# Kernel tuning notes

Measured on AMD Instinct MI355X. Metric: run time of the kernel, lower is better.

## Reference

```python
import jax, jax.numpy as jnp
import numpy as np

TOP_K = 2
NEG_INF = -1e30


def setup_inputs() -> dict:
    key = jax.random.key(0)
    ks = jax.random.split(key, 9)
    S, B, D, H, E, O = 2, 2048, 1024, 2048, 8, 1024
    return {
        "xs": jax.random.normal(ks[0], (S, B, D), jnp.float32),
        "Wg": jax.random.normal(ks[1], (D, E), jnp.float32),
        "b": jax.random.normal(ks[2], (E,), jnp.float32),
        "fc1_w": jax.random.normal(ks[3], (E, H, D), jnp.float32) * 0.02,
        "fc1_b": jax.random.normal(ks[4], (E, H), jnp.float32) * 0.02,
        "fc2_w": jax.random.normal(ks[5], (E, H, H), jnp.float32) * 0.02,
        "fc2_b": jax.random.normal(ks[6], (E, H), jnp.float32) * 0.02,
        "final_w": jax.random.normal(ks[7], (O, H), jnp.float32) * 0.02,
        "final_b": jax.random.normal(ks[8], (O,), jnp.float32) * 0.02,
    }


def reference(xs, Wg, b, fc1_w, fc1_b, fc2_w, fc2_b, final_w, final_b):
    # xs: [S, B, D] stacked x_list
    S = xs.shape[0]
    # gate logits H: [S, B, E]
    Hg = jnp.einsum('sbd,de->sbe', xs, Wg) + b
    expert_probs = jax.nn.softmax(Hg, axis=-1)  # per-view full softmax
    # top-k threshold mask (H >= kth largest value)
    topk_vals = jax.lax.top_k(Hg, TOP_K)[0]          # [S, B, K]
    thr = topk_vals[..., -1:]                         # [S, B, 1]
    H_masked = jnp.where(Hg >= thr, Hg, NEG_INF)
    G = jax.nn.softmax(H_masked, axis=-1)             # [S, B, E]
    # dense all-expert FFN: [S, B, E, H]
    h = jnp.einsum('sbd,ehd->sbeh', xs, fc1_w) + fc1_b
    h = jax.nn.relu(h)
    eo = jnp.einsum('sbeh,egh->sbeg', h, fc2_w) + fc2_b
    # gated sum over experts, averaged over views: [B, H]
    combined = jnp.einsum('sbe,sbeh->bh', G, eo) / S
    out = combined @ final_w.T + final_b               # [B, O]
    return out, expert_probs
```

## Files before the change

kernel.cpp:

```cpp
#include <hip/hip_runtime.h>
#include <stdint.h>

#define S_DIM 2
#define B_DIM 2048
#define D_DIM 1024
#define H_DIM 2048
#define E_DIM 8
#define O_DIM 1024
#define NTOK 4096
#define CAP 12288

typedef __attribute__((ext_vector_type(8))) short bf16x8;
typedef __attribute__((ext_vector_type(4))) float f32x4;

__device__ __forceinline__ unsigned short f2bf(float f) {
    union { float f; uint32_t i; } c; c.f = f;
    uint32_t r = c.i + 0x7FFFu + ((c.i >> 16) & 1u);
    return (unsigned short)(r >> 16);
}
__device__ __forceinline__ float bf2f(unsigned short u) {
    union { uint32_t i; float f; } c; c.i = (uint32_t)u << 16;
    return c.f;
}
__device__ __forceinline__ uint32_t pack2(float a, float b) {
    return (uint32_t)f2bf(a) | ((uint32_t)f2bf(b) << 16);
}
__device__ __forceinline__ void stage8(const float* __restrict__ src,
                                       unsigned short* __restrict__ dst) {
    float4 f0 = *(const float4*)src;
    float4 f1 = *(const float4*)(src + 4);
    int4 v;
    v.x = (int)pack2(f0.x, f0.y);
    v.y = (int)pack2(f0.z, f0.w);
    v.z = (int)pack2(f1.x, f1.y);
    v.w = (int)pack2(f1.z, f1.w);
    *(int4*)dst = v;
}

__device__ __forceinline__ void glds16(const unsigned short* g, unsigned short* l) {
    __builtin_amdgcn_global_load_lds(
        (__attribute__((address_space(1))) void*)g,
        (__attribute__((address_space(3))) void*)l,
        16, 0, 0);
}

__global__ __launch_bounds__(256) void convert_kernel(
    const float* __restrict__ src, unsigned short* __restrict__ dst, int n8)
{
    int i = blockIdx.x * blockDim.x + threadIdx.x;
    if (i < n8) stage8(src + (size_t)i * 8, dst + (size_t)i * 8);
}

__global__ __launch_bounds__(256) void gating_kernel(
    const float* __restrict__ xs,
    const float* __restrict__ Wg,
    const float* __restrict__ bvec,
    float* __restrict__ probs_out,
    int* __restrict__ counts,
    int* __restrict__ sel_cnt,
    int* __restrict__ sel_e,
    float* __restrict__ sel_g,
    unsigned short* __restrict__ xs_bf)
{
    const int wave = threadIdx.x >> 6;
    const int lane = threadIdx.x & 63;
    const int t = blockIdx.x * 4 + wave;
    const float* x = xs + (size_t)t * D_DIM;

    float acc[8];
#pragma unroll
    for (int e = 0; e < 8; ++e) acc[e] = 0.f;

#pragma unroll
    for (int i = 0; i < D_DIM / 64; ++i) {
        int d = i * 64 + lane;
        float xv = x[d];
        xs_bf[(size_t)t * D_DIM + d] = f2bf(xv);
        float4 w0 = *(const float4*)(Wg + (size_t)d * 8);
        float4 w1 = *(const float4*)(Wg + (size_t)d * 8 + 4);
        acc[0] += xv * w0.x; acc[1] += xv * w0.y;
        acc[2] += xv * w0.z; acc[3] += xv * w0.w;
        acc[4] += xv * w1.x; acc[5] += xv * w1.y;
        acc[6] += xv * w1.z; acc[7] += xv * w1.w;
    }
#pragma unroll
    for (int off = 32; off > 0; off >>= 1) {
#pragma unroll
        for (int e = 0; e < 8; ++e)
            acc[e] += __shfl_down(acc[e], off);
    }

    if (lane == 0) {
        float Hg[8];
#pragma unroll
        for (int e = 0; e < 8; ++e) Hg[e] = acc[e] + bvec[e];

        int a1 = 0;
#pragma unroll
        for (int e = 1; e < 8; ++e) if (Hg[e] > Hg[a1]) a1 = e;
        float m1 = Hg[a1];
        float m2 = -1e30f;
#pragma unroll
        for (int e = 0; e < 8; ++e) if (e != a1 && Hg[e] > m2) m2 = Hg[e];

        float ex[8]; float sum = 0.f;
#pragma unroll
        for (int e = 0; e < 8; ++e) { ex[e] = expf(Hg[e] - m1); sum += ex[e]; }
        float inv = 1.f / sum;
#pragma unroll
        for (int e = 0; e < 8; ++e)
            probs_out[(size_t)t * 8 + e] = ex[e] * inv;

        float den = 0.f;
#pragma unroll
        for (int e = 0; e < 8; ++e) if (Hg[e] >= m2) den += ex[e];
        float invd = 1.f / den;
        int n = 0;
#pragma unroll
        for (int e = 0; e < 8; ++e) {
            if (Hg[e] >= m2) {
                sel_e[t * 8 + n] = e;
                sel_g[t * 8 + n] = ex[e] * invd;
                ++n;
                atomicAdd(&counts[e], 1);
            }
        }
        sel_cnt[t] = n;
    }
}

__global__ void scan_kernel(const int* __restrict__ counts, int* __restrict__ offsets)
{
    if (threadIdx.x == 0) {
        int tot = 0;
#pragma unroll
        for (int e = 0; e < 8; ++e) { offsets[e] = tot; tot += counts[e]; }
    }
}

__global__ __launch_bounds__(256) void scatter_kernel(
    const int* __restrict__ sel_cnt,
    const int* __restrict__ sel_e,
    const float* __restrict__ sel_g,
    const int* __restrict__ offsets,
    int* __restrict__ cursors,
    int* __restrict__ pair_token,
    float* __restrict__ pair_gate,
    int* __restrict__ tok_slot)
{
    int t = blockIdx.x * blockDim.x + threadIdx.x;
    if (t >= NTOK) return;
    int n = sel_cnt[t];
    for (int i = 0; i < n && i < 8; ++i) {
        int e = sel_e[t * 8 + i];
        int r = atomicAdd(&cursors[e], 1);
        int slot = offsets[e] + r;
        if (slot < CAP) {
            pair_token[slot] = t;
            pair_gate[slot]  = sel_g[t * 8 + i];
            tok_slot[t * 8 + i] = slot;
        } else {
            tok_slot[t * 8 + i] = -1;
        }
    }
}


__global__ __launch_bounds__(256, 2) void fc1_kernel(
    const unsigned short* __restrict__ xs_bf,
    const unsigned short* __restrict__ fc1_wb,
    const float* __restrict__ fc1_b,
    const int* __restrict__ counts,
    const int* __restrict__ offsets,
    const int* __restrict__ pair_token,
    unsigned short* __restrict__ h)
{
    const int wg = blockIdx.x;
    const int e = wg & 7;
    const int idx = wg >> 3;
    const int mtile = idx >> 3;
    const int ntile = idx & 7;
    const int cnt = counts[e];
    if (mtile * 128 >= cnt) return;
    const int offs = offsets[e];

    __shared__ __align__(16) unsigned short As[128 * 64];
    __shared__ __align__(16) unsigned short Bs[256 * 64];

    const int tid  = threadIdx.x;
    const int lane = tid & 63;
    const int wid  = tid >> 6;
    const int lrow = lane & 15;
    const int kq   = lane >> 4;
    const int swz  = lrow & 7;

    const unsigned short* aSrc[4];
    int aDst[4];
#pragma unroll
    for (int i = 0; i < 4; ++i) {
        int c = i * 256 + tid;
        int row = c >> 3;
        int gran = (c & 7) ^ (row & 7);
        int m = mtile * 128 + row;
        int mc = m < cnt ? m : cnt - 1;
        int tok = pair_token[offs + mc];
        aSrc[i] = xs_bf + (size_t)tok * D_DIM + gran * 8;
        aDst[i] = (i * 256 + wid * 64) * 8;
    }
    const unsigned short* bSrc[8];
    int bDst[8];
#pragma unroll
    for (int i = 0; i < 8; ++i) {
        int c = i * 256 + tid;
        int row = c >> 3;
        int gran = (c & 7) ^ (row & 7);
        int n = ntile * 256 + row;
        bSrc[i] = fc1_wb + ((size_t)e * H_DIM + n) * D_DIM + gran * 8;
        bDst[i] = (i * 256 + wid * 64) * 8;
    }

    f32x4 acc[8][4];
#pragma unroll
    for (int i = 0; i < 8; ++i)
#pragma unroll
        for (int j = 0; j < 4; ++j)
            acc[i][j] = (f32x4){0.f, 0.f, 0.f, 0.f};

    for (int k0 = 0; k0 < D_DIM; k0 += 64) {
        __syncthreads();
#pragma unroll
        for (int i = 0; i < 4; ++i) glds16(aSrc[i] + k0, &As[aDst[i]]);
#pragma unroll
        for (int i = 0; i < 8; ++i) glds16(bSrc[i] + k0, &Bs[bDst[i]]);
        __syncthreads();
#pragma unroll
        for (int ks = 0; ks < 2; ++ks) {
            const int sg = ((ks * 4 + kq) ^ swz) * 8;
            bf16x8 af[8], bfr[4];
#pragma unroll
            for (int i = 0; i < 8; ++i)
                af[i] = *(const bf16x8*)&As[(i * 16 + lrow) * 64 + sg];
#pragma unroll
            for (int j = 0; j < 4; ++j)
                bfr[j] = *(const bf16x8*)&Bs[(wid * 64 + j * 16 + lrow) * 64 + sg];
#pragma unroll
            for (int i = 0; i < 8; ++i)
#pragma unroll
                for (int j = 0; j < 4; ++j)
                    acc[i][j] = __builtin_amdgcn_mfma_f32_16x16x32_bf16(
                        af[i], bfr[j], acc[i][j], 0, 0, 0);
        }
    }

    int ncol[4]; float bias[4];
#pragma unroll
    for (int j = 0; j < 4; ++j) {
        ncol[j] = ntile * 256 + wid * 64 + j * 16 + lrow;
        bias[j] = fc1_b[e * H_DIM + ncol[j]];
    }
#pragma unroll
    for (int i = 0; i < 8; ++i) {
#pragma unroll
        for (int r = 0; r < 4; ++r) {
            int m = mtile * 128 + i * 16 + kq * 4 + r;
            if (m < cnt) {
                size_t base = (size_t)(offs + m) * H_DIM;
#pragma unroll
                for (int j = 0; j < 4; ++j) {
                    float v = acc[i][j][r] + bias[j];
                    h[base + ncol[j]] = f2bf(v > 0.f ? v : 0.f);
                }
            }
        }
    }
}

__global__ __launch_bounds__(256, 2) void fc2_kernel(
    const unsigned short* __restrict__ h,
    const unsigned short* __restrict__ fc2_wb,
    const float* __restrict__ fc2_b,
    const int* __restrict__ counts,
    const int* __restrict__ offsets,
    const float* __restrict__ pair_gate,
    unsigned short* __restrict__ eo_bf)
{
    const int wg = blockIdx.x;
    const int e = wg & 7;
    const int idx = wg >> 3;
    const int mtile = idx >> 3;
    const int ntile = idx & 7;
    const int cnt = counts[e];
    if (mtile * 128 >= cnt) return;
    const int offs = offsets[e];

    __shared__ __align__(16) unsigned short As[128 * 64];
    __shared__ __align__(16) unsigned short Bs[256 * 64];

    const int tid  = threadIdx.x;
    const int lane = tid & 63;
    const int wid  = tid >> 6;
    const int lrow = lane & 15;
    const int kq   = lane >> 4;
    const int swz  = lrow & 7;

    const unsigned short* aSrc[4];
    int aDst[4];
#pragma unroll
    for (int i = 0; i < 4; ++i) {
        int c = i * 256 + tid;
        int row = c >> 3;
        int gran = (c & 7) ^ (row & 7);
        int m = mtile * 128 + row;
        int mc = m < cnt ? m : cnt - 1;
        aSrc[i] = h + (size_t)(offs + mc) * H_DIM + gran * 8;
        aDst[i] = (i * 256 + wid * 64) * 8;
    }
    const unsigned short* bSrc[8];
    int bDst[8];
#pragma unroll
    for (int i = 0; i < 8; ++i) {
        int c = i * 256 + tid;
        int row = c >> 3;
        int gran = (c & 7) ^ (row & 7);
        int n = ntile * 256 + row;
        bSrc[i] = fc2_wb + ((size_t)e * H_DIM + n) * H_DIM + gran * 8;
        bDst[i] = (i * 256 + wid * 64) * 8;
    }

    f32x4 acc[8][4];
#pragma unroll
    for (int i = 0; i < 8; ++i)
#pragma unroll
        for (int j = 0; j < 4; ++j)
            acc[i][j] = (f32x4){0.f, 0.f, 0.f, 0.f};

    for (int k0 = 0; k0 < H_DIM; k0 += 64) {
        __syncthreads();
#pragma unroll
        for (int i = 0; i < 4; ++i) glds16(aSrc[i] + k0, &As[aDst[i]]);
#pragma unroll
        for (int i = 0; i < 8; ++i) glds16(bSrc[i] + k0, &Bs[bDst[i]]);
        __syncthreads();
#pragma unroll
        for (int ks = 0; ks < 2; ++ks) {
            const int sg = ((ks * 4 + kq) ^ swz) * 8;
            bf16x8 af[8], bfr[4];
#pragma unroll
            for (int i = 0; i < 8; ++i)
                af[i] = *(const bf16x8*)&As[(i * 16 + lrow) * 64 + sg];
#pragma unroll
            for (int j = 0; j < 4; ++j)
                bfr[j] = *(const bf16x8*)&Bs[(wid * 64 + j * 16 + lrow) * 64 + sg];
#pragma unroll
            for (int i = 0; i < 8; ++i)
#pragma unroll
                for (int j = 0; j < 4; ++j)
                    acc[i][j] = __builtin_amdgcn_mfma_f32_16x16x32_bf16(
                        af[i], bfr[j], acc[i][j], 0, 0, 0);
        }
    }

    int ncol[4]; float bias[4];
#pragma unroll
    for (int j = 0; j < 4; ++j) {
        ncol[j] = ntile * 256 + wid * 64 + j * 16 + lrow;
        bias[j] = fc2_b[e * H_DIM + ncol[j]];
    }
#pragma unroll
    for (int i = 0; i < 8; ++i) {
#pragma unroll
        for (int r = 0; r < 4; ++r) {
            int m = mtile * 128 + i * 16 + kq * 4 + r;
            if (m < cnt) {
                int slot = offs + m;
                float g  = pair_gate[slot] * 0.5f;
                size_t base = (size_t)slot * H_DIM;
#pragma unroll
                for (int j = 0; j < 4; ++j) {
                    float v = (acc[i][j][r] + bias[j]) * g;
                    eo_bf[base + ncol[j]] = f2bf(v);
                }
            }
        }
    }
}

__global__ __launch_bounds__(256) void reduce_kernel(
    const int* __restrict__ sel_cnt,
    const int* __restrict__ tok_slot,
    const unsigned short* __restrict__ eo_bf,
    unsigned short* __restrict__ combined_bf)
{
    const int b = blockIdx.x;
    const int h0 = threadIdx.x * 8;

    float acc[8];
#pragma unroll
    for (int j = 0; j < 8; ++j) acc[j] = 0.f;

#pragma unroll
    for (int s = 0; s < S_DIM; ++s) {
        int t = s * B_DIM + b;
        int n = sel_cnt[t];
        for (int i = 0; i < n && i < 8; ++i) {
            int slot = tok_slot[t * 8 + i];
            if (slot < 0) continue;
            bf16x8 v = *(const bf16x8*)&eo_bf[(size_t)slot * H_DIM + h0];
#pragma unroll
            for (int j = 0; j < 8; ++j)
                acc[j] += bf2f((unsigned short)v[j]);
        }
    }

    int4 o;
    o.x = (int)pack2(acc[0], acc[1]);
    o.y = (int)pack2(acc[2], acc[3]);
    o.z = (int)pack2(acc[4], acc[5]);
    o.w = (int)pack2(acc[6], acc[7]);
    *(int4*)&combined_bf[(size_t)b * H_DIM + h0] = o;
}

__global__ __launch_bounds__(256) void final_kernel(
    const unsigned short* __restrict__ combined_bf,
    const unsigned short* __restrict__ final_wb,
    const float* __restrict__ final_b,
    float* __restrict__ out)
{
    const int mtile = blockIdx.y;
    const int ntile = blockIdx.x;

    __shared__ __align__(16) unsigned short As[128 * 64];
    __shared__ __align__(16) unsigned short Bs[128 * 64];

    const int tid  = threadIdx.x;
    const int lane = tid & 63;
    const int wave = tid >> 6;
    const int wr = wave >> 1, wc = wave & 1;
    const int lrow = lane & 15;
    const int kq   = lane >> 4;

    const unsigned short* aSrc[4];
    const unsigned short* bSrc[4];
    int dstOff[4];
#pragma unroll
    for (int i = 0; i < 4; ++i) {
        int c = i * 256 + tid;
        int row = c >> 3;
        int gran = (c & 7) ^ (row & 7);
        int m = mtile * 128 + row;
        aSrc[i] = combined_bf + (size_t)m * H_DIM + gran * 8;
        int n = ntile * 128 + row;
        bSrc[i] = final_wb + (size_t)n * H_DIM + gran * 8;
        dstOff[i] = (i * 256 + wave * 64) * 8;
    }

    f32x4 acc[4][4];
#pragma unroll
    for (int i = 0; i < 4; ++i)
#pragma unroll
        for (int j = 0; j < 4; ++j)
            acc[i][j] = (f32x4){0.f, 0.f, 0.f, 0.f};

    for (int k0 = 0; k0 < H_DIM; k0 += 64) {
        __syncthreads();
#pragma unroll
        for (int i = 0; i < 4; ++i) {
            glds16(aSrc[i] + k0, &As[dstOff[i]]);
            glds16(bSrc[i] + k0, &Bs[dstOff[i]]);
        }
        __syncthreads();
#pragma unroll
        for (int ks = 0; ks < 2; ++ks) {
            bf16x8 af[4], bfr[4];
            const int gr = ks * 4 + kq;
            const int sg = (gr ^ (lrow & 7)) * 8;
#pragma unroll
            for (int i = 0; i < 4; ++i) {
                af[i]  = *(const bf16x8*)&As[(wr * 64 + i * 16 + lrow) * 64 + sg];
                bfr[i] = *(const bf16x8*)&Bs[(wc * 64 + i * 16 + lrow) * 64 + sg];
            }
#pragma unroll
            for (int i = 0; i < 4; ++i)
#pragma unroll
                for (int j = 0; j < 4; ++j)
                    acc[i][j] = __builtin_amdgcn_mfma_f32_16x16x32_bf16(af[i], bfr[j], acc[i][j], 0, 0, 0);
        }
    }

    int ncol[4]; float bias[4];
#pragma unroll
    for (int j = 0; j < 4; ++j) {
        ncol[j] = ntile * 128 + wc * 64 + j * 16 + lrow;
        bias[j] = final_b[ncol[j]];
    }
#pragma unroll
    for (int i = 0; i < 4; ++i) {
#pragma unroll
        for (int r = 0; r < 4; ++r) {
            int m = mtile * 128 + wr * 64 + i * 16 + kq * 4 + r;
#pragma unroll
            for (int j = 0; j < 4; ++j)
                out[(size_t)m * O_DIM + ncol[j]] = acc[i][j][r] + bias[j];
        }
    }
}

extern "C" void kernel_launch(void* const* d_in, const int* in_sizes, int n_in,
                              void* d_out, int out_size, void* d_ws, size_t ws_size,
                              hipStream_t stream) {
    const float* xs      = (const float*)d_in[0];
    const float* Wg      = (const float*)d_in[1];
    const float* bvec    = (const float*)d_in[2];
    const float* fc1_w   = (const float*)d_in[3];
    const float* fc1_b   = (const float*)d_in[4];
    const float* fc2_w   = (const float*)d_in[5];
    const float* fc2_b   = (const float*)d_in[6];
    const float* final_w = (const float*)d_in[7];
    const float* final_b = (const float*)d_in[8];

    float* out = (float*)d_out;
    float* probs_out = out + (size_t)B_DIM * O_DIM;

    uint8_t* w = (uint8_t*)d_ws;
    int*   counts     = (int*)(w + 0);
    int*   cursors    = (int*)(w + 64);
    int*   offsets    = (int*)(w + 128);
    int*   sel_cnt    = (int*)(w + 256);
    int*   sel_e      = (int*)(w + 0x5000);
    float* sel_g      = (float*)(w + 0x25000);
    int*   pair_token = (int*)(w + 0x45000);
    float* pair_gate  = (float*)(w + 0x51000);
    int*   tok_slot   = (int*)(w + 0x5D000);
    unsigned short* h = (unsigned short*)(w + 0x1060000);
    unsigned short* xs_bf   = (unsigned short*)(w + 0x4060000);
    unsigned short* fc1_wb  = (unsigned short*)(w + 0x4860000);
    unsigned short* fc2_wb  = (unsigned short*)(w + 0x6860000);
    unsigned short* final_wb    = (unsigned short*)(w + 0xA860000);
    unsigned short* combined_bf = (unsigned short*)(w + 0xAC60000);
    unsigned short* eo_bf       = (unsigned short*)(w + 0xB460000);

    hipMemsetAsync(w, 0, 256, stream);

    convert_kernel<<<(E_DIM * H_DIM * D_DIM / 8) / 256, 256, 0, stream>>>(
        fc1_w, fc1_wb, E_DIM * H_DIM * D_DIM / 8);
    convert_kernel<<<(E_DIM * H_DIM * H_DIM / 8) / 256, 256, 0, stream>>>(
        fc2_w, fc2_wb, E_DIM * H_DIM * H_DIM / 8);
    convert_kernel<<<(O_DIM * H_DIM / 8) / 256, 256, 0, stream>>>(
        final_w, final_wb, O_DIM * H_DIM / 8);

    gating_kernel<<<NTOK / 4, 256, 0, stream>>>(xs, Wg, bvec, probs_out,
                                                counts, sel_cnt, sel_e, sel_g, xs_bf);
    scan_kernel<<<1, 64, 0, stream>>>(counts, offsets);
    scatter_kernel<<<NTOK / 256, 256, 0, stream>>>(sel_cnt, sel_e, sel_g, offsets,
                                                   cursors, pair_token, pair_gate,
                                                   tok_slot);
    fc1_kernel<<<E_DIM * (NTOK / 128) * (H_DIM / 256), 256, 0, stream>>>(
        xs_bf, fc1_wb, fc1_b, counts, offsets, pair_token, h);
    fc2_kernel<<<E_DIM * (NTOK / 128) * (H_DIM / 256), 256, 0, stream>>>(
        h, fc2_wb, fc2_b, counts, offsets, pair_gate, eo_bf);
    reduce_kernel<<<B_DIM, 256, 0, stream>>>(sel_cnt, tok_slot, eo_bf, combined_bf);
    final_kernel<<<dim3(O_DIM / 128, B_DIM / 128), 256, 0, stream>>>(
        combined_bf, final_wb, final_b, out);
}
```

Measured before the change: 638.4 us.

## Merge weight conversions and scan into fewer launches; shrink fc1 tile to 128x128

The three fp32-to-bf16 weight conversion launches and the workspace memset are merged into one kernel. The one-thread scan kernel is folded into the scatter kernel, where each block computes the expert offsets into shared memory. The fc1 GEMM drops from 128x256 tiles to 128x128 tiles on a 2x2 wave grid, which doubles the number of workgroups and cuts accumulator registers. The intent is to remove launch overhead and improve fc1 occupancy, at the cost of fetching more A tiles in fc1. Zeroing the counters inside the conversion kernel relies on stream ordering before the gating kernel, which holds.

```diff
diff --git a/kernel.cpp b/kernel.cpp
--- a/kernel.cpp
+++ b/kernel.cpp
@@ -44,11 +44,31 @@
         16, 0, 0);
 }
 
-__global__ __launch_bounds__(256) void convert_kernel(
-    const float* __restrict__ src, unsigned short* __restrict__ dst, int n8)
-{
-    int i = blockIdx.x * blockDim.x + threadIdx.x;
-    if (i < n8) stage8(src + (size_t)i * 8, dst + (size_t)i * 8);
+#define N8_FC1   ((size_t)E_DIM * H_DIM * D_DIM / 8)
+#define N8_FC2   ((size_t)E_DIM * H_DIM * H_DIM / 8)
+#define N8_FINAL ((size_t)O_DIM * H_DIM / 8)
+#define N8_TOTAL (N8_FC1 + N8_FC2 + N8_FINAL)
+
+__global__ __launch_bounds__(256) void convert_all_kernel(
+    const float* __restrict__ fc1_w,
+    const float* __restrict__ fc2_w,
+    const float* __restrict__ final_w,
+    unsigned short* __restrict__ fc1_wb,
+    unsigned short* __restrict__ fc2_wb,
+    unsigned short* __restrict__ final_wb,
+    int* __restrict__ ws_zero)
+{
+    if (blockIdx.x == 0 && threadIdx.x < 64) ws_zero[threadIdx.x] = 0;
+    size_t i = (size_t)blockIdx.x * blockDim.x + threadIdx.x;
+    if (i < N8_FC1) {
+        stage8(fc1_w + i * 8, fc1_wb + i * 8);
+    } else if (i < N8_FC1 + N8_FC2) {
+        size_t j = i - N8_FC1;
+        stage8(fc2_w + j * 8, fc2_wb + j * 8);
+    } else if (i < N8_TOTAL) {
+        size_t j = i - N8_FC1 - N8_FC2;
+        stage8(final_w + j * 8, final_wb + j * 8);
+    }
 }
 
 __global__ __launch_bounds__(256) void gating_kernel(
@@ -129,32 +149,36 @@
     }
 }
 
-__global__ void scan_kernel(const int* __restrict__ counts, int* __restrict__ offsets)
-{
-    if (threadIdx.x == 0) {
-        int tot = 0;
-#pragma unroll
-        for (int e = 0; e < 8; ++e) { offsets[e] = tot; tot += counts[e]; }
-    }
-}
-
 __global__ __launch_bounds__(256) void scatter_kernel(
     const int* __restrict__ sel_cnt,
     const int* __restrict__ sel_e,
     const float* __restrict__ sel_g,
-    const int* __restrict__ offsets,
+    const int* __restrict__ counts,
+    int* __restrict__ offsets,
     int* __restrict__ cursors,
     int* __restrict__ pair_token,
     float* __restrict__ pair_gate,
     int* __restrict__ tok_slot)
 {
+    __shared__ int offs_s[8];
+    if (threadIdx.x == 0) {
+        int tot = 0;
+#pragma unroll
+        for (int e = 0; e < 8; ++e) { offs_s[e] = tot; tot += counts[e]; }
+        if (blockIdx.x == 0) {
+#pragma unroll
+            for (int e = 0; e < 8; ++e) offsets[e] = offs_s[e];
+        }
+    }
+    __syncthreads();
+
     int t = blockIdx.x * blockDim.x + threadIdx.x;
     if (t >= NTOK) return;
     int n = sel_cnt[t];
     for (int i = 0; i < n && i < 8; ++i) {
         int e = sel_e[t * 8 + i];
         int r = atomicAdd(&cursors[e], 1);
-        int slot = offsets[e] + r;
+        int slot = offs_s[e] + r;
         if (slot < CAP) {
             pair_token[slot] = t;
             pair_gate[slot]  = sel_g[t * 8 + i];
@@ -165,8 +189,7 @@
     }
 }
 
-
-__global__ __launch_bounds__(256, 2) void fc1_kernel(
+__global__ __launch_bounds__(256) void fc1_kernel(
     const unsigned short* __restrict__ xs_bf,
     const unsigned short* __restrict__ fc1_wb,
     const float* __restrict__ fc1_b,
@@ -178,24 +201,25 @@
     const int wg = blockIdx.x;
     const int e = wg & 7;
     const int idx = wg >> 3;
-    const int mtile = idx >> 3;
-    const int ntile = idx & 7;
+    const int mtile = idx >> 4;
+    const int ntile = idx & 15;
     const int cnt = counts[e];
     if (mtile * 128 >= cnt) return;
     const int offs = offsets[e];
 
     __shared__ __align__(16) unsigned short As[128 * 64];
-    __shared__ __align__(16) unsigned short Bs[256 * 64];
+    __shared__ __align__(16) unsigned short Bs[128 * 64];
 
     const int tid  = threadIdx.x;
     const int lane = tid & 63;
-    const int wid  = tid >> 6;
+    const int wave = tid >> 6;
+    const int wr = wave >> 1, wc = wave & 1;
     const int lrow = lane & 15;
     const int kq   = lane >> 4;
-    const int swz  = lrow & 7;
 
     const unsigned short* aSrc[4];
-    int aDst[4];
+    const unsigned short* bSrc[4];
+    int dstOff[4];
 #pragma unroll
     for (int i = 0; i < 4; ++i) {
         int c = i * 256 + tid;
@@ -205,23 +229,14 @@
         int mc = m < cnt ? m : cnt - 1;
         int tok = pair_token[offs + mc];
         aSrc[i] = xs_bf + (size_t)tok * D_DIM + gran * 8;
-        aDst[i] = (i * 256 + wid * 64) * 8;
-    }
-    const unsigned short* bSrc[8];
-    int bDst[8];
-#pragma unroll
-    for (int i = 0; i < 8; ++i) {
-        int c = i * 256 + tid;
-        int row = c >> 3;
-        int gran = (c & 7) ^ (row & 7);
-        int n = ntile * 256 + row;
+        int n = ntile * 128 + row;
         bSrc[i] = fc1_wb + ((size_t)e * H_DIM + n) * D_DIM + gran * 8;
-        bDst[i] = (i * 256 + wid * 64) * 8;
-    }
-
-    f32x4 acc[8][4];
-#pragma unroll
-    for (int i = 0; i < 8; ++i)
+        dstOff[i] = (i * 256 + wave * 64) * 8;
+    }
+
+    f32x4 acc[4][4];
+#pragma unroll
+    for (int i = 0; i < 4; ++i)
 #pragma unroll
         for (int j = 0; j < 4; ++j)
             acc[i][j] = (f32x4){0.f, 0.f, 0.f, 0.f};
@@ -229,40 +244,40 @@
     for (int k0 = 0; k0 < D_DIM; k0 += 64) {
         __syncthreads();
 #pragma unroll
-        for (int i = 0; i < 4; ++i) glds16(aSrc[i] + k0, &As[aDst[i]]);
-#pragma unroll
-        for (int i = 0; i < 8; ++i) glds16(bSrc[i] + k0, &Bs[bDst[i]]);
+        for (int i = 0; i < 4; ++i) {
+            glds16(aSrc[i] + k0, &As[dstOff[i]]);
+            glds16(bSrc[i] + k0, &Bs[dstOff[i]]);
+        }
         __syncthreads();
 #pragma unroll
         for (int ks = 0; ks < 2; ++ks) {
-            const int sg = ((ks * 4 + kq) ^ swz) * 8;
-            bf16x8 af[8], bfr[4];
-#pragma unroll
-            for (int i = 0; i < 8; ++i)
-                af[i] = *(const bf16x8*)&As[(i * 16 + lrow) * 64 + sg];
-#pragma unroll
-            for (int j = 0; j < 4; ++j)
-                bfr[j] = *(const bf16x8*)&Bs[(wid * 64 + j * 16 + lrow) * 64 + sg];
-#pragma unroll
-            for (int i = 0; i < 8; ++i)
+            bf16x8 af[4], bfr[4];
+            const int gr = ks * 4 + kq;
+            const int sg = (gr ^ (lrow & 7)) * 8;
+#pragma unroll
+            for (int i = 0; i < 4; ++i) {
+                af[i]  = *(const bf16x8*)&As[(wr * 64 + i * 16 + lrow) * 64 + sg];
+                bfr[i] = *(const bf16x8*)&Bs[(wc * 64 + i * 16 + lrow) * 64 + sg];
+            }
+#pragma unroll
+            for (int i = 0; i < 4; ++i)
 #pragma unroll
                 for (int j = 0; j < 4; ++j)
-                    acc[i][j] = __builtin_amdgcn_mfma_f32_16x16x32_bf16(
-                        af[i], bfr[j], acc[i][j], 0, 0, 0);
+                    acc[i][j] = __builtin_amdgcn_mfma_f32_16x16x32_bf16(af[i], bfr[j], acc[i][j], 0, 0, 0);
         }
     }
 
     int ncol[4]; float bias[4];
 #pragma unroll
     for (int j = 0; j < 4; ++j) {
-        ncol[j] = ntile * 256 + wid * 64 + j * 16 + lrow;
+        ncol[j] = ntile * 128 + wc * 64 + j * 16 + lrow;
         bias[j] = fc1_b[e * H_DIM + ncol[j]];
     }
 #pragma unroll
-    for (int i = 0; i < 8; ++i) {
+    for (int i = 0; i < 4; ++i) {
 #pragma unroll
         for (int r = 0; r < 4; ++r) {
-            int m = mtile * 128 + i * 16 + kq * 4 + r;
+            int m = mtile * 128 + wr * 64 + i * 16 + kq * 4 + r;
             if (m < cnt) {
                 size_t base = (size_t)(offs + m) * H_DIM;
 #pragma unroll
@@ -539,26 +554,24 @@
     unsigned short* combined_bf = (unsigned short*)(w + 0xAC60000);
     unsigned short* eo_bf       = (unsigned short*)(w + 0xB460000);
 
-    hipMemsetAsync(w, 0, 256, stream);
-
-    convert_kernel<<<(E_DIM * H_DIM * D_DIM / 8) / 256, 256, 0, stream>>>(
-        fc1_w, fc1_wb, E_DIM * H_DIM * D_DIM / 8);
-    convert_kernel<<<(E_DIM * H_DIM * H_DIM / 8) / 256, 256, 0, stream>>>(
-        fc2_w, fc2_wb, E_DIM * H_DIM * H_DIM / 8);
-    convert_kernel<<<(O_DIM * H_DIM / 8) / 256, 256, 0, stream>>>(
-        final_w, final_wb, O_DIM * H_DIM / 8);
+    convert_all_kernel<<<(int)(N8_TOTAL / 256), 256, 0, stream>>>(
+        fc1_w, fc2_w, final_w, fc1_wb, fc2_wb, final_wb, (int*)w);
 
     gating_kernel<<<NTOK / 4, 256, 0, stream>>>(xs, Wg, bvec, probs_out,
                                                 counts, sel_cnt, sel_e, sel_g, xs_bf);
-    scan_kernel<<<1, 64, 0, stream>>>(counts, offsets);
-    scatter_kernel<<<NTOK / 256, 256, 0, stream>>>(sel_cnt, sel_e, sel_g, offsets,
-                                                   cursors, pair_token, pair_gate,
-                                                   tok_slot);
-    fc1_kernel<<<E_DIM * (NTOK / 128) * (H_DIM / 256), 256, 0, stream>>>(
+
+    scatter_kernel<<<NTOK / 256, 256, 0, stream>>>(sel_cnt, sel_e, sel_g,
+                                                   counts, offsets, cursors,
+                                                   pair_token, pair_gate, tok_slot);
+
+    fc1_kernel<<<E_DIM * (NTOK / 128) * (H_DIM / 128), 256, 0, stream>>>(
         xs_bf, fc1_wb, fc1_b, counts, offsets, pair_token, h);
+
     fc2_kernel<<<E_DIM * (NTOK / 128) * (H_DIM / 256), 256, 0, stream>>>(
         h, fc2_wb, fc2_b, counts, offsets, pair_gate, eo_bf);
+
     reduce_kernel<<<B_DIM, 256, 0, stream>>>(sel_cnt, tok_slot, eo_bf, combined_bf);
+
     final_kernel<<<dim3(O_DIM / 128, B_DIM / 128), 256, 0, stream>>>(
         combined_bf, final_wb, final_b, out);
 }
```

Result: no change. 628.8 us (-1.5%).
